# Optimization experiments

Measured on AMD Instinct MI355X. Metric: run time of the kernel, lower is better.

The kernel has to match this reference:

```python
import jax, jax.numpy as jnp
import numpy as np

N = 100_000   # nodes
E = 200_000   # directed edges
G = 2_500     # graphs in batch
F_NODE = 16
F_EDGE = 8
H1 = 32
H2 = 16


def setup_inputs() -> dict:
    key = jax.random.key(0)
    ks = jax.random.split(key, 24)
    p = lambda k, shape: 0.1 * jax.random.normal(k, shape, dtype=jnp.float32)
    inp = {
        "x": jax.random.normal(ks[0], (N, F_NODE), dtype=jnp.float32),
        "edge_attr": jax.random.normal(ks[1], (E, F_EDGE), dtype=jnp.float32),
        # edge-MLP for conv1: F_EDGE -> 16 -> F_NODE*H1
        "w_e1a": p(ks[2], (F_EDGE, 16)), "b_e1a": p(ks[3], (16,)),
        "w_e1b": p(ks[4], (16, F_NODE * H1)), "b_e1b": p(ks[5], (F_NODE * H1,)),
        "w_root1": p(ks[6], (F_NODE, H1)), "b_root1": p(ks[7], (H1,)),
        # edge-MLP for conv2: F_EDGE -> 16 -> H1*H2
        "w_e2a": p(ks[8], (F_EDGE, 16)), "b_e2a": p(ks[9], (16,)),
        "w_e2b": p(ks[10], (16, H1 * H2)), "b_e2b": p(ks[11], (H1 * H2,)),
        "w_root2": p(ks[12], (H1, H2)), "b_root2": p(ks[13], (H2,)),
        # attention-pool gate nn: F_NODE -> F_NODE -> 1
        "w_g1": p(ks[14], (F_NODE, F_NODE)), "b_g1": p(ks[15], (F_NODE,)),
        "w_g2": p(ks[16], (F_NODE, 1)), "b_g2": p(ks[17], (1,)),
        # head: (H2 + F_NODE) -> 8 -> 1
        "w_l1": p(ks[18], (H2 + F_NODE, 8)), "b_l1": p(ks[19], (8,)),
        "w_l2": p(ks[20], (8, 1)), "b_l2": p(ks[21], (1,)),
        "edge_index": jax.random.randint(ks[22], (2, E), 0, N),
        "batch": jnp.sort(jax.random.randint(ks[23], (N,), 0, G)),
    }
    return inp


def _nnconv(x, src, tgt, edge_attr, wa, ba, wb, bb, wr, br, in_c, out_c, n):
    # PyG NNConv: x_i' = x_i @ W_root + b + sum_{j->i} x_j @ Theta(e_ji)
    h = jax.nn.relu(edge_attr @ wa + ba)              # [E, 16]
    theta = (h @ wb + bb).reshape(-1, in_c, out_c)    # [E, in, out]
    msg = jnp.einsum('ei,eio->eo', x[src], theta)     # [E, out]
    agg = jax.ops.segment_sum(msg, tgt, num_segments=n)
    return x @ wr + br + agg


def reference(x, edge_attr, w_e1a, b_e1a, w_e1b, b_e1b, w_root1, b_root1,
              w_e2a, b_e2a, w_e2b, b_e2b, w_root2, b_root2,
              w_g1, b_g1, w_g2, b_g2, w_l1, b_l1, w_l2, b_l2,
              edge_index, batch):
    src, tgt = edge_index[0], edge_index[1]
    n = x.shape[0]

    # GlobalAttention pooling on raw node features (per-graph segment softmax)
    gate = jax.nn.relu(x @ w_g1 + b_g1) @ w_g2 + b_g2          # [N, 1]
    m = jax.ops.segment_max(gate, batch, num_segments=G)       # [G, 1]
    a = jnp.exp(gate - m[batch])
    s = jax.ops.segment_sum(a, batch, num_segments=G)
    x_att = jax.ops.segment_sum((a / s[batch]) * x, batch, num_segments=G)  # [G, F_NODE]

    # Two NNConv layers with ReLU
    h = jax.nn.relu(_nnconv(x, src, tgt, edge_attr, w_e1a, b_e1a, w_e1b, b_e1b,
                            w_root1, b_root1, F_NODE, H1, n))
    h = jax.nn.relu(_nnconv(h, src, tgt, edge_attr, w_e2a, b_e2a, w_e2b, b_e2b,
                            w_root2, b_root2, H1, H2, n))

    # global_mean_pool
    cnt = jax.ops.segment_sum(jnp.ones((n, 1), h.dtype), batch, num_segments=G)
    mean = jax.ops.segment_sum(h, batch, num_segments=G) / jnp.maximum(cnt, 1.0)

    z = jnp.concatenate([mean, x_att], axis=1)  # [G, H2 + F_NODE]
    # eval mode: dropout p=0.5 is identity; two linear layers, no activation between
    z = z @ w_l1 + b_l1
    z = z @ w_l2 + b_l2
    return z
```

## Files before the change

### kernel.cpp

```cpp
#include <hip/hip_runtime.h>
#include <hip/hip_bf16.h>

#define NN 100000
#define NE 200000
#define NG 2500
#define FN 16
#define FE 8
#define H1C 32
#define H2C 16
#define KH 16

typedef __attribute__((ext_vector_type(4))) float f32x4;
typedef _Float16 __attribute__((ext_vector_type(2))) half2v;
typedef _Float16 __attribute__((ext_vector_type(8))) half8v;
typedef __fp16 __attribute__((ext_vector_type(2))) pkf16x2;

__device__ __forceinline__ float bf2f(unsigned int u){
  union { unsigned int i; float f; } v; v.i = (u & 0xffffu) << 16; return v.f;
}
__device__ __forceinline__ unsigned int pkh(float a, float b){
  union { pkf16x2 h; unsigned int u; } v; v.h = __builtin_amdgcn_cvt_pkrtz(a, b); return v.u;
}
__device__ __forceinline__ float h2lo(unsigned int u){
  union { unsigned short s; _Float16 h; } v; v.s = (unsigned short)u; return (float)v.h;
}
__device__ __forceinline__ float h2hi(unsigned int u){
  union { unsigned short s; _Float16 h; } v; v.s = (unsigned short)(u >> 16); return (float)v.h;
}
__device__ __forceinline__ float rdf(const void* p, long i, bool isbf){
  return isbf ? bf2f(((const unsigned short*)p)[i]) : ((const float*)p)[i];
}
__device__ __forceinline__ void atomic_pk_f16(unsigned short* addr, unsigned int pk){
  asm volatile("global_atomic_pk_add_f16 %0, %1, off" :: "v"(addr), "v"(pk) : "memory");
}
__device__ __forceinline__ bool detect_isbf(const void* __restrict__ x){
  const unsigned short* u = (const unsigned short*)x;
  int lane = threadIdx.x & 63;
  float f = bf2f(u[2*lane]);
  float a = fabsf(f);
  bool sane = (f == 0.0f) || (a > 1e-4f && a < 1e4f);
  unsigned long long b = __ballot(sane);
  return __popcll(b) >= 32;
}
__device__ __forceinline__ void load_x16(const void* __restrict__ xin, bool isbf, int n, float* xv){
  if(isbf){
    uint4 u0 = ((const uint4*)xin)[2*n], u1 = ((const uint4*)xin)[2*n+1];
    xv[0]=bf2f(u0.x); xv[1]=bf2f(u0.x>>16); xv[2]=bf2f(u0.y); xv[3]=bf2f(u0.y>>16);
    xv[4]=bf2f(u0.z); xv[5]=bf2f(u0.z>>16); xv[6]=bf2f(u0.w); xv[7]=bf2f(u0.w>>16);
    xv[8]=bf2f(u1.x); xv[9]=bf2f(u1.x>>16); xv[10]=bf2f(u1.y); xv[11]=bf2f(u1.y>>16);
    xv[12]=bf2f(u1.z); xv[13]=bf2f(u1.z>>16); xv[14]=bf2f(u1.w); xv[15]=bf2f(u1.w>>16);
  } else {
    #pragma unroll
    for(int q = 0; q < 4; q++){
      float4 v = ((const float4*)xin)[4*n + q];
      xv[q*4+0]=v.x; xv[q*4+1]=v.y; xv[q*4+2]=v.z; xv[q*4+3]=v.w;
    }
  }
}

#define NW 20
struct WArgs { const void* p[NW]; };
enum {
  OW_E1A=0,     OB_E1A=128,   OW_E1B=144,   OB_E1B=8336,  OW_R1=8848,  OB_R1=9360,
  OW_E2A=9392,  OB_E2A=9520,  OW_E2B=9536,  OB_E2B=17728, OW_R2=18240, OB_R2=18752,
  OW_G1=18768,  OB_G1=19024,  OW_G2=19040,  OB_G2=19056,
  OW_L1=19057,  OB_L1=19313,  OW_L2=19321,  OB_L2=19329
};

template<int IN, int OUT, bool RAWX>
__device__ __forceinline__ void conv_tile(
    int u, const void* __restrict__ nodef, bool isbf,
    const unsigned int* __restrict__ hpk, const int* __restrict__ ei,
    const unsigned short* __restrict__ wpack, unsigned short* __restrict__ agg)
{
  constexpr int KMF  = ((KH*IN + IN + 31)/32)*32;
  constexpr int KP   = KMF + 8;
  constexpr int NT   = OUT/16;
  constexpr int KS   = KMF/32;
  int tid = threadIdx.x;
  int lane = tid & 63, m = lane & 15, quad = lane >> 4;
  int wid = tid >> 6;
  int ebase = u*64 + wid*16;
  int em = ebase + m;
  int sn = ei[em];
  int q1 = quad >> 1;
  int xoff = (IN == 16) ? ((quad & 1)*8) : (quad*8);
  union { half8v v; half2v h[4]; unsigned int w[4]; } X;
  if(RAWX){
    if(isbf){
      uint4 uu = *(const uint4*)((const unsigned short*)nodef + (size_t)sn*IN + xoff);
      X.w[0] = pkh(bf2f(uu.x), bf2f(uu.x >> 16));
      X.w[1] = pkh(bf2f(uu.y), bf2f(uu.y >> 16));
      X.w[2] = pkh(bf2f(uu.z), bf2f(uu.z >> 16));
      X.w[3] = pkh(bf2f(uu.w), bf2f(uu.w >> 16));
    } else {
      const float4* xp = (const float4*)((const float*)nodef + (size_t)sn*IN + xoff);
      float4 v0 = xp[0], v1 = xp[1];
      X.w[0] = pkh(v0.x, v0.y);
      X.w[1] = pkh(v0.z, v0.w);
      X.w[2] = pkh(v1.x, v1.y);
      X.w[3] = pkh(v1.z, v1.w);
    }
  } else {
    uint4 uu = *(const uint4*)((const unsigned short*)nodef + (size_t)sn*IN + xoff);
    X.w[0]=uu.x; X.w[1]=uu.y; X.w[2]=uu.z; X.w[3]=uu.w;
  }
  unsigned int hu[8];
  {
    const uint4* hp = (const uint4*)(hpk + (size_t)em*8);
    uint4 u0 = hp[0], u1 = hp[1];
    hu[0]=u0.x; hu[1]=u0.y; hu[2]=u0.z; hu[3]=u0.w;
    hu[4]=u1.x; hu[5]=u1.y; hu[6]=u1.z; hu[7]=u1.w;
  }
  int4 tg = *(const int4*)(ei + NE + ebase + quad*4);

  f32x4 acc[NT];
  #pragma unroll
  for(int nt = 0; nt < NT; nt++) acc[nt] = (f32x4){0.f,0.f,0.f,0.f};

  const half8v hz = {};
  #pragma unroll
  for(int ks = 0; ks < KS; ks++){
    union { half8v v; half2v h[4]; } A;
    if(ks < KS-1){
      unsigned short hs = (unsigned short)((IN == 16) ? (hu[ks] >> (16*q1))
                                                      : (hu[ks >> 1] >> (16*(ks & 1))));
      union { unsigned short s; _Float16 h; } hc; hc.s = hs;
      half2v hv2 = { hc.h, hc.h };
      #pragma unroll
      for(int k = 0; k < 4; k++) A.h[k] = hv2 * X.h[k];
    } else {
      if(IN == 16) A.v = (quad < 2) ? X.v : hz;
      else         A.v = X.v;
    }
    #pragma unroll
    for(int nt = 0; nt < NT; nt++){
      half8v b = *(const half8v*)(wpack + (size_t)(nt*16 + m)*KP + ks*32 + quad*8);
      acc[nt] = __builtin_amdgcn_mfma_f32_16x16x32_f16(A.v, b, acc[nt], 0, 0, 0);
    }
  }
  int tr[4] = {tg.x, tg.y, tg.z, tg.w};
  int mlo = m & ~1;
  bool evn = (m & 1) == 0;
  #pragma unroll
  for(int r = 0; r < 4; r++){
    #pragma unroll
    for(int nt = 0; nt < NT; nt++){
      float v = acc[nt][r];
      float vn = __shfl_xor(v, 1);
      if(evn ? (r < 2) : (r >= 2)){
        unsigned int pk = evn ? pkh(v, vn) : pkh(vn, v);
        atomic_pk_f16(agg + (size_t)tr[r]*OUT + nt*16 + mlo, pk);
      }
    }
  }
}

#define MB_A 76
#define MB_B (MB_A + 19)
#define MB_C (MB_B + 18)
#define MB_D (MB_C + 391)
#define MB_E (MB_D + 782)
#define MB_F (MB_E + 391)
__global__ void __launch_bounds__(256) mega1_kernel(
    const void* __restrict__ xin, const void* __restrict__ efin, WArgs w,
    const int* __restrict__ batch,
    float* __restrict__ wts, unsigned int* __restrict__ wpack1, unsigned int* __restrict__ wpack2,
    float* __restrict__ gate,
    unsigned int* __restrict__ hpk1,
    int* __restrict__ gstart, unsigned short* __restrict__ agg1)
{
  int b = blockIdx.x, tid = threadIdx.x;
  if(b < MB_A){
    bool isbf = detect_isbf(xin);
    int i = b*256 + tid;
    if(i >= 19330) return;
    const int sz[NW] = {128,16,8192,512,512,32, 128,16,8192,512,512,16, 256,16,16,1, 256,8,8,1};
    int seg = 0; long base = 0;
    while(i - base >= sz[seg]){ base += sz[seg]; seg++; }
    wts[i] = rdf(w.p[seg], i - base, isbf);
    return;
  }
  if(b < MB_B){
    bool isbf = detect_isbf(xin);
    int j = (b - MB_A)*256 + tid;
    if(j >= 4736) return;
    int n = j / 148; int k = (j % 148) * 2;
    float v0 = 0.f, v1 = 0.f;
    if(k < 256)        v0 = rdf(w.p[2], (long)k*32 + n, isbf);
    else if(k < 272)   v0 = rdf(w.p[3], (long)(k-256)*32 + n, isbf);
    if(k+1 < 256)      v1 = rdf(w.p[2], (long)(k+1)*32 + n, isbf);
    else if(k+1 < 272) v1 = rdf(w.p[3], (long)(k+1-256)*32 + n, isbf);
    wpack1[j] = pkh(v0, v1);
    return;
  }
  if(b < MB_C){
    bool isbf = detect_isbf(xin);
    int j = (b - MB_B)*256 + tid;
    if(j >= 4416) return;
    int n = j / 276; int k = (j % 276) * 2;
    float v0 = 0.f, v1 = 0.f;
    if(k < 512)        v0 = rdf(w.p[8], (long)k*16 + n, isbf);
    else if(k < 544)   v0 = rdf(w.p[9], (long)(k-512)*16 + n, isbf);
    if(k+1 < 512)      v1 = rdf(w.p[8], (long)(k+1)*16 + n, isbf);
    else if(k+1 < 544) v1 = rdf(w.p[9], (long)(k+1-512)*16 + n, isbf);
    wpack2[j] = pkh(v0, v1);
    return;
  }
  if(b < MB_D){
    __shared__ float s_w1[FN*FN], s_b1[FN], s_w2[FN], s_b2v[1];
    bool isbf = detect_isbf(xin);
    if(tid < FN*FN) s_w1[tid] = rdf(w.p[12], tid, isbf);
    if(tid < FN){ s_b1[tid] = rdf(w.p[13], tid, isbf); s_w2[tid] = rdf(w.p[14], tid, isbf); }
    if(tid == 0) s_b2v[0] = rdf(w.p[15], 0, isbf);
    __syncthreads();
    int n = (b - MB_C)*256 + tid;
    if(n >= NN) return;
    {
      int b1 = batch[n];
      int b0 = (n == 0) ? -1 : batch[n-1];
      for(int g2 = b0 + 1; g2 <= b1; g2++) gstart[g2] = n;
      if(n == NN-1) for(int g2 = b1 + 1; g2 <= NG; g2++) gstart[g2] = NN;
    }
    float xv[FN];
    load_x16(xin, isbf, n, xv);
    float g = s_b2v[0];
    #pragma unroll
    for(int j = 0; j < FN; j++){
      float hj = s_b1[j];
      #pragma unroll
      for(int i = 0; i < FN; i++) hj += xv[i] * s_w1[i*FN + j];
      hj = hj > 0.f ? hj : 0.f;
      g += hj * s_w2[j];
    }
    gate[n] = g;
    return;
  }
  if(b < MB_E){
    __shared__ float s_w1[FE*KH], s_b1[KH];
    bool isbf = detect_isbf(xin);
    if(tid < FE*KH) s_w1[tid] = rdf(w.p[0], tid, isbf);
    if(tid < KH) s_b1[tid] = rdf(w.p[1], tid, isbf);
    __syncthreads();
    int e = (b - MB_D)*256 + tid;
    if(e >= NE) return;
    float ev[FE];
    if(isbf){
      uint4 u = ((const uint4*)efin)[e];
      ev[0]=bf2f(u.x); ev[1]=bf2f(u.x>>16); ev[2]=bf2f(u.y); ev[3]=bf2f(u.y>>16);
      ev[4]=bf2f(u.z); ev[5]=bf2f(u.z>>16); ev[6]=bf2f(u.w); ev[7]=bf2f(u.w>>16);
    } else {
      float4 a = ((const float4*)efin)[2*e], bb = ((const float4*)efin)[2*e+1];
      ev[0]=a.x; ev[1]=a.y; ev[2]=a.z; ev[3]=a.w; ev[4]=bb.x; ev[5]=bb.y; ev[6]=bb.z; ev[7]=bb.w;
    }
    unsigned int o[8];
    #pragma unroll
    for(int d = 0; d < 8; d++){
      float h0 = s_b1[2*d], h1 = s_b1[2*d+1];
      #pragma unroll
      for(int k = 0; k < FE; k++){
        h0 += ev[k] * s_w1[k*KH + 2*d];
        h1 += ev[k] * s_w1[k*KH + 2*d+1];
      }
      h0 = h0 > 0.f ? h0 : 0.f; h1 = h1 > 0.f ? h1 : 0.f;
      o[d] = pkh(h0, h1);
    }
    uint4* p1 = (uint4*)(hpk1 + (size_t)e*8);
    p1[0] = make_uint4(o[0],o[1],o[2],o[3]); p1[1] = make_uint4(o[4],o[5],o[6],o[7]);
    return;
  }
  {
    int idx = (b - MB_E)*256 + tid;
    if(idx < 100000){
      uint4 z = make_uint4(0,0,0,0);
      uint4* p = (uint4*)((char*)agg1 + (size_t)idx*64);
      p[0] = z; p[1] = z; p[2] = z; p[3] = z;
    }
  }
}

#define C1_CONV (NE/64)
#define C1_E2   (C1_CONV + 782)
#define C1_Z    (C1_E2 + 196)
#define C1_ATT  (C1_Z + 625)
__global__ void __launch_bounds__(256) conv1_kernel(
    const void* __restrict__ xin, const void* __restrict__ efin,
    const float* __restrict__ wts,
    const unsigned int* __restrict__ hpk1, const int* __restrict__ ei,
    const unsigned short* __restrict__ wpack1,
    unsigned short* __restrict__ agg1, unsigned short* __restrict__ agg2,
    unsigned int* __restrict__ hpk2,
    const float* __restrict__ gate, const int* __restrict__ gstart,
    float* __restrict__ xatt)
{
  int b = blockIdx.x, tid = threadIdx.x;
  bool isbf = detect_isbf(xin);
  if(b < C1_CONV){
    conv_tile<FN, H1C, true>(b, xin, isbf, hpk1, ei, wpack1, agg1);
    return;
  }
  if(b < C1_E2){
    __shared__ float s_w2[FE*KH], s_b2[KH];
    if(tid < FE*KH) s_w2[tid] = wts[OW_E2A + tid];
    if(tid < KH) s_b2[tid] = wts[OB_E2A + tid];
    __syncthreads();
    int e = (b - C1_CONV)*256 + tid;
    if(e >= NE) return;
    float ev[FE];
    if(isbf){
      uint4 u = ((const uint4*)efin)[e];
      ev[0]=bf2f(u.x); ev[1]=bf2f(u.x>>16); ev[2]=bf2f(u.y); ev[3]=bf2f(u.y>>16);
      ev[4]=bf2f(u.z); ev[5]=bf2f(u.z>>16); ev[6]=bf2f(u.w); ev[7]=bf2f(u.w>>16);
    } else {
      float4 a = ((const float4*)efin)[2*e], bb = ((const float4*)efin)[2*e+1];
      ev[0]=a.x; ev[1]=a.y; ev[2]=a.z; ev[3]=a.w; ev[4]=bb.x; ev[5]=bb.y; ev[6]=bb.z; ev[7]=bb.w;
    }
    unsigned int o[8];
    #pragma unroll
    for(int d = 0; d < 8; d++){
      float h0 = s_b2[2*d], h1 = s_b2[2*d+1];
      #pragma unroll
      for(int k = 0; k < FE; k++){
        h0 += ev[k] * s_w2[k*KH + 2*d];
        h1 += ev[k] * s_w2[k*KH + 2*d+1];
      }
      h0 = h0 > 0.f ? h0 : 0.f; h1 = h1 > 0.f ? h1 : 0.f;
      o[d] = pkh(h0, h1);
    }
    uint4* p2 = (uint4*)(hpk2 + (size_t)e*8);
    p2[0] = make_uint4(o[0],o[1],o[2],o[3]); p2[1] = make_uint4(o[4],o[5],o[6],o[7]);
    return;
  }
  if(b < C1_Z){
    int idx = (b - C1_E2)*256 + tid;
    if(idx < 50000){
      uint4 z = make_uint4(0,0,0,0);
      uint4* p = (uint4*)((char*)agg2 + (size_t)idx*64);
      p[0] = z; p[1] = z; p[2] = z; p[3] = z;
    }
    return;
  }
  {
    int lane = tid & 63, wid = tid >> 6;
    int g = (b - C1_Z)*4 + wid;
    int start = gstart[g], end = gstart[g+1];
    float mx = -1e30f;
    for(int n = start + lane; n < end; n += 64) mx = fmaxf(mx, gate[n]);
    #pragma unroll
    for(int o = 32; o >= 1; o >>= 1) mx = fmaxf(mx, __shfl_xor(mx, o));
    float s = 0.f;
    float acc[FN];
    #pragma unroll
    for(int f = 0; f < FN; f++) acc[f] = 0.f;
    for(int n = start + lane; n < end; n += 64){
      float a = __expf(gate[n] - mx);
      s += a;
      float xv[FN];
      load_x16(xin, isbf, n, xv);
      #pragma unroll
      for(int f = 0; f < FN; f++) acc[f] += a * xv[f];
    }
    #pragma unroll
    for(int o = 32; o >= 1; o >>= 1){
      s += __shfl_xor(s, o);
      #pragma unroll
      for(int f = 0; f < FN; f++) acc[f] += __shfl_xor(acc[f], o);
    }
    if(lane < FN) xatt[(size_t)g*FN + lane] = (end > start && s > 0.f) ? acc[lane] / s : 0.f;
  }
}

__global__ void __launch_bounds__(256) conv2_kernel(
    const unsigned short* __restrict__ h1b, const unsigned int* __restrict__ hpk2,
    const int* __restrict__ ei, const unsigned short* __restrict__ wpack2,
    unsigned short* __restrict__ agg2)
{
  conv_tile<H1C, H2C, false>(blockIdx.x, h1b, false, hpk2, ei, wpack2, agg2);
}

__global__ void __launch_bounds__(256) node1_kernel(
    const void* __restrict__ xin, const unsigned short* __restrict__ agg1,
    const float* __restrict__ wr, const float* __restrict__ br,
    unsigned short* __restrict__ h1b)
{
  __shared__ float s_w[FN*H1C], s_b[H1C];
  for(int i = threadIdx.x; i < FN*H1C; i += 256) s_w[i] = wr[i];
  if(threadIdx.x < H1C) s_b[threadIdx.x] = br[threadIdx.x];
  bool isbf = detect_isbf(xin);
  __syncthreads();
  int g = blockIdx.x*256 + threadIdx.x;
  int n = g >> 3, q = g & 7;
  if(n >= NN) return;
  uint2 au = *(const uint2*)(agg1 + (size_t)n*H1C + q*4);
  float a0 = s_b[q*4+0] + h2lo(au.x), a1 = s_b[q*4+1] + h2hi(au.x);
  float a2 = s_b[q*4+2] + h2lo(au.y), a3 = s_b[q*4+3] + h2hi(au.y);
  float xv[FN];
  load_x16(xin, isbf, n, xv);
  #pragma unroll
  for(int i = 0; i < FN; i++){
    float xi = xv[i];
    a0 += xi*s_w[i*H1C + q*4+0]; a1 += xi*s_w[i*H1C + q*4+1];
    a2 += xi*s_w[i*H1C + q*4+2]; a3 += xi*s_w[i*H1C + q*4+3];
  }
  a0 = a0>0.f?a0:0.f; a1 = a1>0.f?a1:0.f; a2 = a2>0.f?a2:0.f; a3 = a3>0.f?a3:0.f;
  uint2 hb; hb.x = pkh(a0, a1); hb.y = pkh(a2, a3);
  *(uint2*)(h1b + (size_t)n*H1C + q*4) = hb;
}

__global__ void __launch_bounds__(256) node2_kernel(
    const unsigned short* __restrict__ h1b, const unsigned short* __restrict__ agg2,
    const float* __restrict__ wr, const float* __restrict__ br, float* __restrict__ h2)
{
  __shared__ float s_w[H1C*H2C], s_b[H2C];
  for(int i = threadIdx.x; i < H1C*H2C; i += 256) s_w[i] = wr[i];
  if(threadIdx.x < H2C) s_b[threadIdx.x] = br[threadIdx.x];
  __syncthreads();
  int g = blockIdx.x*256 + threadIdx.x;
  int n = g >> 2, q = g & 3;
  if(n >= NN) return;
  uint2 au = *(const uint2*)(agg2 + (size_t)n*H2C + q*4);
  float a0 = s_b[q*4+0] + h2lo(au.x), a1 = s_b[q*4+1] + h2hi(au.x);
  float a2 = s_b[q*4+2] + h2lo(au.y), a3 = s_b[q*4+3] + h2hi(au.y);
  const unsigned int* hb = (const unsigned int*)(h1b + (size_t)n*H1C);
  #pragma unroll
  for(int i2 = 0; i2 < H1C/2; i2++){
    unsigned int u = hb[i2];
    float x0 = h2lo(u), x1 = h2hi(u);
    int i = 2*i2;
    a0 += x0*s_w[i*H2C + q*4+0] + x1*s_w[(i+1)*H2C + q*4+0];
    a1 += x0*s_w[i*H2C + q*4+1] + x1*s_w[(i+1)*H2C + q*4+1];
    a2 += x0*s_w[i*H2C + q*4+2] + x1*s_w[(i+1)*H2C + q*4+2];
    a3 += x0*s_w[i*H2C + q*4+3] + x1*s_w[(i+1)*H2C + q*4+3];
  }
  float4 r; r.x = a0>0.f?a0:0.f; r.y = a1>0.f?a1:0.f; r.z = a2>0.f?a2:0.f; r.w = a3>0.f?a3:0.f;
  *(float4*)(h2 + (size_t)n*H2C + q*4) = r;
}

__global__ void head_kernel(const float* __restrict__ xatt,
    const float* __restrict__ h2, const int* __restrict__ gstart, const void* __restrict__ xin,
    const float* __restrict__ wl1, const float* __restrict__ bl1,
    const float* __restrict__ wl2, const float* __restrict__ bl2,
    void* __restrict__ out)
{
  __shared__ float sz[H2C + FN];
  int g = blockIdx.x;
  int lane = threadIdx.x;
  bool isbf = detect_isbf(xin);
  int start = gstart[g];
  int end   = gstart[g + 1];
  float acc[H2C];
  #pragma unroll
  for(int f = 0; f < H2C; f++) acc[f] = 0.f;
  for(int n = start + lane; n < end; n += 64){
    const float4* hp = (const float4*)(h2 + (size_t)n*H2C);
    #pragma unroll
    for(int q = 0; q < 4; q++){
      float4 v = hp[q];
      acc[q*4+0] += v.x; acc[q*4+1] += v.y; acc[q*4+2] += v.z; acc[q*4+3] += v.w;
    }
  }
  #pragma unroll
  for(int o = 32; o >= 1; o >>= 1){
    #pragma unroll
    for(int f = 0; f < H2C; f++) acc[f] += __shfl_xor(acc[f], o);
  }
  float inv = 1.f / fmaxf((float)(end - start), 1.f);
  if(lane < H2C) sz[lane] = acc[lane] * inv;
  if(lane < FN)  sz[H2C + lane] = xatt[(size_t)g*FN + lane];
  __syncthreads();
  if(lane == 0){
    float t1[8];
    #pragma unroll
    for(int j = 0; j < 8; j++){
      float t = bl1[j];
      #pragma unroll
      for(int c = 0; c < H2C + FN; c++) t += sz[c] * wl1[c*8 + j];
      t1[j] = t;
    }
    float o = bl2[0];
    #pragma unroll
    for(int j = 0; j < 8; j++) o += t1[j] * wl2[j];
    if(isbf) ((__hip_bfloat16*)out)[g] = __float2bfloat16(o);
    else     ((float*)out)[g] = o;
  }
}

extern "C" void kernel_launch(void* const* d_in, const int* in_sizes, int n_in,
                              void* d_out, int out_size, void* d_ws, size_t ws_size,
                              hipStream_t stream)
{
  const int* ei    = (const int*)d_in[22];
  const int* batch = (const int*)d_in[23];

  float* ws = (float*)d_ws;
  float* gate   = ws;
  float* wts    = gate + 100000;
  float* xatt   = wts + 19360;
  int*   gstart = (int*)(xatt + 40000);
  unsigned int* wpack1 = (unsigned int*)(gstart + 2504);
  unsigned int* wpack2 = wpack1 + 4736;
  unsigned int* hpk1   = wpack2 + 4416;
  unsigned int* hpk2   = hpk1 + 1600000;
  unsigned short* h1b  = (unsigned short*)(hpk2 + 1600000);
  float* h2     = (float*)(h1b + 3200000);
  unsigned short* agg1 = (unsigned short*)(h2 + 1600000);
  unsigned short* agg2 = agg1 + 3200000;

  WArgs wa;
  for(int i = 0; i < NW; i++) wa.p[i] = d_in[2 + i];

  mega1_kernel<<<MB_F, 256, 0, stream>>>(d_in[0], d_in[1], wa, batch,
      wts, wpack1, wpack2, gate, hpk1, gstart, agg1);

  conv1_kernel<<<C1_ATT, 256, 0, stream>>>(d_in[0], d_in[1], wts, hpk1, ei,
      (const unsigned short*)wpack1, agg1, agg2, hpk2, gate, gstart, xatt);
  node1_kernel<<<(NN*8 + 255)/256, 256, 0, stream>>>(d_in[0], agg1, wts+OW_R1, wts+OB_R1, h1b);

  conv2_kernel<<<NE/64, 256, 0, stream>>>(h1b, hpk2, ei,
      (const unsigned short*)wpack2, agg2);
  node2_kernel<<<(NN*4 + 255)/256, 256, 0, stream>>>(h1b, agg2, wts+OW_R2, wts+OB_R2, h2);

  head_kernel<<<NG, 64, 0, stream>>>(xatt, h2, gstart, d_in[0],
      wts+OW_L1, wts+OB_L1, wts+OW_L2, wts+OB_L2, d_out);
}
```

Baseline: 185.0 us.

## Fuse node-update kernels into conv2 gather and head pooling

Removes the node1 and node2 kernels. conv2 now recomputes the layer-1 node update (root linear, bias, ReLU) for each source node it gathers, using raw x and agg1. The head kernel recomputes both node updates per node during mean pooling and handles four graphs per block. This cuts two launches and the h1b/h2 intermediate buffers, at the price of redundant per-edge and per-node arithmetic and larger register use.

```diff
diff --git a/kernel.cpp b/kernel.cpp
--- a/kernel.cpp
+++ b/kernel.cpp
@@ -66,95 +66,6 @@
   OW_G1=18768,  OB_G1=19024,  OW_G2=19040,  OB_G2=19056,
   OW_L1=19057,  OB_L1=19313,  OW_L2=19321,  OB_L2=19329
 };
-
-template<int IN, int OUT, bool RAWX>
-__device__ __forceinline__ void conv_tile(
-    int u, const void* __restrict__ nodef, bool isbf,
-    const unsigned int* __restrict__ hpk, const int* __restrict__ ei,
-    const unsigned short* __restrict__ wpack, unsigned short* __restrict__ agg)
-{
-  constexpr int KMF  = ((KH*IN + IN + 31)/32)*32;
-  constexpr int KP   = KMF + 8;
-  constexpr int NT   = OUT/16;
-  constexpr int KS   = KMF/32;
-  int tid = threadIdx.x;
-  int lane = tid & 63, m = lane & 15, quad = lane >> 4;
-  int wid = tid >> 6;
-  int ebase = u*64 + wid*16;
-  int em = ebase + m;
-  int sn = ei[em];
-  int q1 = quad >> 1;
-  int xoff = (IN == 16) ? ((quad & 1)*8) : (quad*8);
-  union { half8v v; half2v h[4]; unsigned int w[4]; } X;
-  if(RAWX){
-    if(isbf){
-      uint4 uu = *(const uint4*)((const unsigned short*)nodef + (size_t)sn*IN + xoff);
-      X.w[0] = pkh(bf2f(uu.x), bf2f(uu.x >> 16));
-      X.w[1] = pkh(bf2f(uu.y), bf2f(uu.y >> 16));
-      X.w[2] = pkh(bf2f(uu.z), bf2f(uu.z >> 16));
-      X.w[3] = pkh(bf2f(uu.w), bf2f(uu.w >> 16));
-    } else {
-      const float4* xp = (const float4*)((const float*)nodef + (size_t)sn*IN + xoff);
-      float4 v0 = xp[0], v1 = xp[1];
-      X.w[0] = pkh(v0.x, v0.y);
-      X.w[1] = pkh(v0.z, v0.w);
-      X.w[2] = pkh(v1.x, v1.y);
-      X.w[3] = pkh(v1.z, v1.w);
-    }
-  } else {
-    uint4 uu = *(const uint4*)((const unsigned short*)nodef + (size_t)sn*IN + xoff);
-    X.w[0]=uu.x; X.w[1]=uu.y; X.w[2]=uu.z; X.w[3]=uu.w;
-  }
-  unsigned int hu[8];
-  {
-    const uint4* hp = (const uint4*)(hpk + (size_t)em*8);
-    uint4 u0 = hp[0], u1 = hp[1];
-    hu[0]=u0.x; hu[1]=u0.y; hu[2]=u0.z; hu[3]=u0.w;
-    hu[4]=u1.x; hu[5]=u1.y; hu[6]=u1.z; hu[7]=u1.w;
-  }
-  int4 tg = *(const int4*)(ei + NE + ebase + quad*4);
-
-  f32x4 acc[NT];
-  #pragma unroll
-  for(int nt = 0; nt < NT; nt++) acc[nt] = (f32x4){0.f,0.f,0.f,0.f};
-
-  const half8v hz = {};
-  #pragma unroll
-  for(int ks = 0; ks < KS; ks++){
-    union { half8v v; half2v h[4]; } A;
-    if(ks < KS-1){
-      unsigned short hs = (unsigned short)((IN == 16) ? (hu[ks] >> (16*q1))
-                                                      : (hu[ks >> 1] >> (16*(ks & 1))));
-      union { unsigned short s; _Float16 h; } hc; hc.s = hs;
-      half2v hv2 = { hc.h, hc.h };
-      #pragma unroll
-      for(int k = 0; k < 4; k++) A.h[k] = hv2 * X.h[k];
-    } else {
-      if(IN == 16) A.v = (quad < 2) ? X.v : hz;
-      else         A.v = X.v;
-    }
-    #pragma unroll
-    for(int nt = 0; nt < NT; nt++){
-      half8v b = *(const half8v*)(wpack + (size_t)(nt*16 + m)*KP + ks*32 + quad*8);
-      acc[nt] = __builtin_amdgcn_mfma_f32_16x16x32_f16(A.v, b, acc[nt], 0, 0, 0);
-    }
-  }
-  int tr[4] = {tg.x, tg.y, tg.z, tg.w};
-  int mlo = m & ~1;
-  bool evn = (m & 1) == 0;
-  #pragma unroll
-  for(int r = 0; r < 4; r++){
-    #pragma unroll
-    for(int nt = 0; nt < NT; nt++){
-      float v = acc[nt][r];
-      float vn = __shfl_xor(v, 1);
-      if(evn ? (r < 2) : (r >= 2)){
-        unsigned int pk = evn ? pkh(v, vn) : pkh(vn, v);
-        atomic_pk_f16(agg + (size_t)tr[r]*OUT + nt*16 + mlo, pk);
-      }
-    }
-  }
-}
 
 #define MB_A 76
 #define MB_B (MB_A + 19)
@@ -287,7 +198,7 @@
     const void* __restrict__ xin, const void* __restrict__ efin,
     const float* __restrict__ wts,
     const unsigned int* __restrict__ hpk1, const int* __restrict__ ei,
-    const unsigned short* __restrict__ wpack1,
+    const unsigned short* __restrict__ wpack,
     unsigned short* __restrict__ agg1, unsigned short* __restrict__ agg2,
     unsigned int* __restrict__ hpk2,
     const float* __restrict__ gate, const int* __restrict__ gstart,
@@ -296,7 +207,75 @@
   int b = blockIdx.x, tid = threadIdx.x;
   bool isbf = detect_isbf(xin);
   if(b < C1_CONV){
-    conv_tile<FN, H1C, true>(b, xin, isbf, hpk1, ei, wpack1, agg1);
+    constexpr int IN = FN, OUT = H1C;
+    constexpr int KMF = 288, KP = 296, NT = 2, KS = 9;
+    int lane = tid & 63, m = lane & 15, quad = lane >> 4;
+    int wid = tid >> 6;
+    int ebase = b*64 + wid*16;
+    int em = ebase + m;
+    int sn = ei[em];
+    int q1 = quad >> 1;
+    int xoff = (quad & 1)*8;
+    union { half8v v; half2v h[4]; unsigned int w[4]; } X;
+    if(isbf){
+      uint4 uu = *(const uint4*)((const unsigned short*)xin + (size_t)sn*IN + xoff);
+      X.w[0] = pkh(bf2f(uu.x), bf2f(uu.x >> 16));
+      X.w[1] = pkh(bf2f(uu.y), bf2f(uu.y >> 16));
+      X.w[2] = pkh(bf2f(uu.z), bf2f(uu.z >> 16));
+      X.w[3] = pkh(bf2f(uu.w), bf2f(uu.w >> 16));
+    } else {
+      const float4* xp = (const float4*)((const float*)xin + (size_t)sn*IN + xoff);
+      float4 v0 = xp[0], v1 = xp[1];
+      X.w[0] = pkh(v0.x, v0.y);
+      X.w[1] = pkh(v0.z, v0.w);
+      X.w[2] = pkh(v1.x, v1.y);
+      X.w[3] = pkh(v1.z, v1.w);
+    }
+    unsigned int hu[8];
+    {
+      const uint4* hp = (const uint4*)(hpk1 + (size_t)em*8);
+      uint4 u0 = hp[0], u1 = hp[1];
+      hu[0]=u0.x; hu[1]=u0.y; hu[2]=u0.z; hu[3]=u0.w;
+      hu[4]=u1.x; hu[5]=u1.y; hu[6]=u1.z; hu[7]=u1.w;
+    }
+    int4 tg = *(const int4*)(ei + NE + ebase + quad*4);
+    f32x4 acc[NT];
+    #pragma unroll
+    for(int nt = 0; nt < NT; nt++) acc[nt] = (f32x4){0.f,0.f,0.f,0.f};
+    const half8v hz = {};
+    #pragma unroll
+    for(int ks = 0; ks < KS; ks++){
+      union { half8v v; half2v h[4]; } A;
+      if(ks < KS-1){
+        unsigned short hs = (unsigned short)(hu[ks] >> (16*q1));
+        union { unsigned short s; _Float16 h; } hc; hc.s = hs;
+        half2v hv2 = { hc.h, hc.h };
+        #pragma unroll
+        for(int k = 0; k < 4; k++) A.h[k] = hv2 * X.h[k];
+      } else {
+        A.v = (quad < 2) ? X.v : hz;
+      }
+      #pragma unroll
+      for(int nt = 0; nt < NT; nt++){
+        half8v bb = *(const half8v*)(wpack + (size_t)(nt*16 + m)*KP + ks*32 + quad*8);
+        acc[nt] = __builtin_amdgcn_mfma_f32_16x16x32_f16(A.v, bb, acc[nt], 0, 0, 0);
+      }
+    }
+    int tr[4] = {tg.x, tg.y, tg.z, tg.w};
+    int mlo = m & ~1;
+    bool evn = (m & 1) == 0;
+    #pragma unroll
+    for(int r = 0; r < 4; r++){
+      #pragma unroll
+      for(int nt = 0; nt < NT; nt++){
+        float v = acc[nt][r];
+        float vn = __shfl_xor(v, 1);
+        if(evn ? (r < 2) : (r >= 2)){
+          unsigned int pk = evn ? pkh(v, vn) : pkh(vn, v);
+          atomic_pk_f16(agg1 + (size_t)tr[r]*H1C + nt*16 + mlo, pk);
+        }
+      }
+    }
     return;
   }
   if(b < C1_E2){
@@ -371,93 +350,153 @@
 }
 
 __global__ void __launch_bounds__(256) conv2_kernel(
-    const unsigned short* __restrict__ h1b, const unsigned int* __restrict__ hpk2,
-    const int* __restrict__ ei, const unsigned short* __restrict__ wpack2,
-    unsigned short* __restrict__ agg2)
+    const void* __restrict__ xin, const unsigned short* __restrict__ agg1,
+    const float* __restrict__ wts,
+    const unsigned int* __restrict__ hpk2, const int* __restrict__ ei,
+    const unsigned short* __restrict__ wpack, unsigned short* __restrict__ agg2)
 {
-  conv_tile<H1C, H2C, false>(blockIdx.x, h1b, false, hpk2, ei, wpack2, agg2);
-}
-
-__global__ void __launch_bounds__(256) node1_kernel(
-    const void* __restrict__ xin, const unsigned short* __restrict__ agg1,
-    const float* __restrict__ wr, const float* __restrict__ br,
-    unsigned short* __restrict__ h1b)
-{
+  constexpr int KP = 552, KS = 17;
   __shared__ float s_w[FN*H1C], s_b[H1C];
-  for(int i = threadIdx.x; i < FN*H1C; i += 256) s_w[i] = wr[i];
-  if(threadIdx.x < H1C) s_b[threadIdx.x] = br[threadIdx.x];
+  int tid = threadIdx.x;
+  for(int i = tid; i < FN*H1C; i += 256) s_w[i] = wts[OW_R1 + i];
+  if(tid < H1C) s_b[tid] = wts[OB_R1 + tid];
   bool isbf = detect_isbf(xin);
   __syncthreads();
-  int g = blockIdx.x*256 + threadIdx.x;
-  int n = g >> 3, q = g & 7;
-  if(n >= NN) return;
-  uint2 au = *(const uint2*)(agg1 + (size_t)n*H1C + q*4);
-  float a0 = s_b[q*4+0] + h2lo(au.x), a1 = s_b[q*4+1] + h2hi(au.x);
-  float a2 = s_b[q*4+2] + h2lo(au.y), a3 = s_b[q*4+3] + h2hi(au.y);
+  int lane = tid & 63, m = lane & 15, quad = lane >> 4;
+  int wid = tid >> 6;
+  int ebase = blockIdx.x*64 + wid*16;
+  int em = ebase + m;
+  int sn = ei[em];
+  int xoff = quad*8;
   float xv[FN];
-  load_x16(xin, isbf, n, xv);
+  load_x16(xin, isbf, sn, xv);
+  uint4 au = *(const uint4*)(agg1 + (size_t)sn*H1C + xoff);
+  float hv[8];
+  hv[0]=h2lo(au.x); hv[1]=h2hi(au.x); hv[2]=h2lo(au.y); hv[3]=h2hi(au.y);
+  hv[4]=h2lo(au.z); hv[5]=h2hi(au.z); hv[6]=h2lo(au.w); hv[7]=h2hi(au.w);
+  #pragma unroll
+  for(int t = 0; t < 8; t++) hv[t] += s_b[xoff + t];
   #pragma unroll
   for(int i = 0; i < FN; i++){
     float xi = xv[i];
-    a0 += xi*s_w[i*H1C + q*4+0]; a1 += xi*s_w[i*H1C + q*4+1];
-    a2 += xi*s_w[i*H1C + q*4+2]; a3 += xi*s_w[i*H1C + q*4+3];
-  }
-  a0 = a0>0.f?a0:0.f; a1 = a1>0.f?a1:0.f; a2 = a2>0.f?a2:0.f; a3 = a3>0.f?a3:0.f;
-  uint2 hb; hb.x = pkh(a0, a1); hb.y = pkh(a2, a3);
-  *(uint2*)(h1b + (size_t)n*H1C + q*4) = hb;
-}
-
-__global__ void __launch_bounds__(256) node2_kernel(
-    const unsigned short* __restrict__ h1b, const unsigned short* __restrict__ agg2,
-    const float* __restrict__ wr, const float* __restrict__ br, float* __restrict__ h2)
-{
-  __shared__ float s_w[H1C*H2C], s_b[H2C];
-  for(int i = threadIdx.x; i < H1C*H2C; i += 256) s_w[i] = wr[i];
-  if(threadIdx.x < H2C) s_b[threadIdx.x] = br[threadIdx.x];
-  __syncthreads();
-  int g = blockIdx.x*256 + threadIdx.x;
-  int n = g >> 2, q = g & 3;
-  if(n >= NN) return;
-  uint2 au = *(const uint2*)(agg2 + (size_t)n*H2C + q*4);
-  float a0 = s_b[q*4+0] + h2lo(au.x), a1 = s_b[q*4+1] + h2hi(au.x);
-  float a2 = s_b[q*4+2] + h2lo(au.y), a3 = s_b[q*4+3] + h2hi(au.y);
-  const unsigned int* hb = (const unsigned int*)(h1b + (size_t)n*H1C);
-  #pragma unroll
-  for(int i2 = 0; i2 < H1C/2; i2++){
-    unsigned int u = hb[i2];
-    float x0 = h2lo(u), x1 = h2hi(u);
-    int i = 2*i2;
-    a0 += x0*s_w[i*H2C + q*4+0] + x1*s_w[(i+1)*H2C + q*4+0];
-    a1 += x0*s_w[i*H2C + q*4+1] + x1*s_w[(i+1)*H2C + q*4+1];
-    a2 += x0*s_w[i*H2C + q*4+2] + x1*s_w[(i+1)*H2C + q*4+2];
-    a3 += x0*s_w[i*H2C + q*4+3] + x1*s_w[(i+1)*H2C + q*4+3];
-  }
-  float4 r; r.x = a0>0.f?a0:0.f; r.y = a1>0.f?a1:0.f; r.z = a2>0.f?a2:0.f; r.w = a3>0.f?a3:0.f;
-  *(float4*)(h2 + (size_t)n*H2C + q*4) = r;
-}
-
-__global__ void head_kernel(const float* __restrict__ xatt,
-    const float* __restrict__ h2, const int* __restrict__ gstart, const void* __restrict__ xin,
-    const float* __restrict__ wl1, const float* __restrict__ bl1,
-    const float* __restrict__ wl2, const float* __restrict__ bl2,
+    #pragma unroll
+    for(int t = 0; t < 8; t++) hv[t] += xi * s_w[i*H1C + xoff + t];
+  }
+  union { half8v v; half2v h[4]; unsigned int w[4]; } X;
+  #pragma unroll
+  for(int k = 0; k < 4; k++){
+    float a = hv[2*k]   > 0.f ? hv[2*k]   : 0.f;
+    float b = hv[2*k+1] > 0.f ? hv[2*k+1] : 0.f;
+    X.w[k] = pkh(a, b);
+  }
+  unsigned int hu[8];
+  {
+    const uint4* hp = (const uint4*)(hpk2 + (size_t)em*8);
+    uint4 u0 = hp[0], u1 = hp[1];
+    hu[0]=u0.x; hu[1]=u0.y; hu[2]=u0.z; hu[3]=u0.w;
+    hu[4]=u1.x; hu[5]=u1.y; hu[6]=u1.z; hu[7]=u1.w;
+  }
+  int4 tg = *(const int4*)(ei + NE + ebase + quad*4);
+  f32x4 acc = (f32x4){0.f,0.f,0.f,0.f};
+  #pragma unroll
+  for(int ks = 0; ks < KS; ks++){
+    union { half8v v; half2v h[4]; } A;
+    if(ks < KS-1){
+      unsigned short hs = (unsigned short)(hu[ks >> 1] >> (16*(ks & 1)));
+      union { unsigned short s; _Float16 h; } hc; hc.s = hs;
+      half2v hv2 = { hc.h, hc.h };
+      #pragma unroll
+      for(int k = 0; k < 4; k++) A.h[k] = hv2 * X.h[k];
+    } else {
+      A.v = X.v;
+    }
+    half8v bb = *(const half8v*)(wpack + (size_t)m*KP + ks*32 + quad*8);
+    acc = __builtin_amdgcn_mfma_f32_16x16x32_f16(A.v, bb, acc, 0, 0, 0);
+  }
+  int tr[4] = {tg.x, tg.y, tg.z, tg.w};
+  int mlo = m & ~1;
+  bool evn = (m & 1) == 0;
+  #pragma unroll
+  for(int r = 0; r < 4; r++){
+    float v = acc[r];
+    float vn = __shfl_xor(v, 1);
+    if(evn ? (r < 2) : (r >= 2)){
+      unsigned int pk = evn ? pkh(v, vn) : pkh(vn, v);
+      atomic_pk_f16(agg2 + (size_t)tr[r]*H2C + mlo, pk);
+    }
+  }
+}
+
+__global__ void __launch_bounds__(256) head_kernel(
+    const void* __restrict__ xin, const unsigned short* __restrict__ agg1,
+    const unsigned short* __restrict__ agg2, const float* __restrict__ xatt,
+    const int* __restrict__ gstart, const float* __restrict__ wts,
     void* __restrict__ out)
 {
-  __shared__ float sz[H2C + FN];
-  int g = blockIdx.x;
-  int lane = threadIdx.x;
+  __shared__ float s_w1[FN*H1C], s_b1[H1C], s_w2[H1C*H2C], s_b2[H2C];
+  __shared__ float s_l1[(H2C+FN)*8], s_lb1[8], s_l2[8], s_lb2[1];
+  __shared__ float sz[4][H2C+FN];
+  int tid = threadIdx.x;
+  for(int i = tid; i < FN*H1C; i += 256){ s_w1[i] = wts[OW_R1+i]; s_w2[i] = wts[OW_R2+i]; }
+  if(tid < H1C) s_b1[tid] = wts[OB_R1+tid];
+  if(tid < H2C) s_b2[tid] = wts[OB_R2+tid];
+  s_l1[tid] = wts[OW_L1 + tid];
+  if(tid < 8){ s_lb1[tid] = wts[OB_L1+tid]; s_l2[tid] = wts[OW_L2+tid]; }
+  if(tid == 0) s_lb2[0] = wts[OB_L2];
   bool isbf = detect_isbf(xin);
-  int start = gstart[g];
-  int end   = gstart[g + 1];
+  __syncthreads();
+  int lane = tid & 63, wid = tid >> 6;
+  int g = blockIdx.x*4 + wid;
+  int start = gstart[g], end = gstart[g+1];
   float acc[H2C];
   #pragma unroll
   for(int f = 0; f < H2C; f++) acc[f] = 0.f;
   for(int n = start + lane; n < end; n += 64){
-    const float4* hp = (const float4*)(h2 + (size_t)n*H2C);
-    #pragma unroll
-    for(int q = 0; q < 4; q++){
-      float4 v = hp[q];
-      acc[q*4+0] += v.x; acc[q*4+1] += v.y; acc[q*4+2] += v.z; acc[q*4+3] += v.w;
-    }
+    float xv[FN];
+    load_x16(xin, isbf, n, xv);
+    float h1[H1C];
+    {
+      const uint4* ap = (const uint4*)(agg1 + (size_t)n*H1C);
+      uint4 a0 = ap[0], a1 = ap[1], a2 = ap[2], a3 = ap[3];
+      unsigned int aw[16] = {a0.x,a0.y,a0.z,a0.w, a1.x,a1.y,a1.z,a1.w,
+                             a2.x,a2.y,a2.z,a2.w, a3.x,a3.y,a3.z,a3.w};
+      #pragma unroll
+      for(int c2 = 0; c2 < 16; c2++){ h1[2*c2] = h2lo(aw[c2]); h1[2*c2+1] = h2hi(aw[c2]); }
+    }
+    #pragma unroll
+    for(int c = 0; c < H1C; c++) h1[c] += s_b1[c];
+    #pragma unroll
+    for(int i = 0; i < FN; i++){
+      float xi = xv[i];
+      #pragma unroll
+      for(int c = 0; c < H1C; c++) h1[c] += xi * s_w1[i*H1C + c];
+    }
+    #pragma unroll
+    for(int c2 = 0; c2 < 16; c2++){
+      float a = h1[2*c2]   > 0.f ? h1[2*c2]   : 0.f;
+      float b = h1[2*c2+1] > 0.f ? h1[2*c2+1] : 0.f;
+      unsigned int u = pkh(a, b);
+      h1[2*c2] = h2lo(u); h1[2*c2+1] = h2hi(u);
+    }
+    float hv2[H2C];
+    {
+      const uint4* bp = (const uint4*)(agg2 + (size_t)n*H2C);
+      uint4 b0 = bp[0], b1 = bp[1];
+      unsigned int bw[8] = {b0.x,b0.y,b0.z,b0.w, b1.x,b1.y,b1.z,b1.w};
+      #pragma unroll
+      for(int o2 = 0; o2 < 8; o2++){ hv2[2*o2] = h2lo(bw[o2]); hv2[2*o2+1] = h2hi(bw[o2]); }
+    }
+    #pragma unroll
+    for(int o = 0; o < H2C; o++) hv2[o] += s_b2[o];
+    #pragma unroll
+    for(int i2 = 0; i2 < H1C/2; i2++){
+      float x0 = h1[2*i2], x1 = h1[2*i2+1];
+      #pragma unroll
+      for(int o = 0; o < H2C; o++)
+        hv2[o] += x0*s_w2[2*i2*H2C + o] + x1*s_w2[(2*i2+1)*H2C + o];
+    }
+    #pragma unroll
+    for(int o = 0; o < H2C; o++) acc[o] += (hv2[o] > 0.f ? hv2[o] : 0.f);
   }
   #pragma unroll
   for(int o = 32; o >= 1; o >>= 1){
@@ -465,21 +504,21 @@
     for(int f = 0; f < H2C; f++) acc[f] += __shfl_xor(acc[f], o);
   }
   float inv = 1.f / fmaxf((float)(end - start), 1.f);
-  if(lane < H2C) sz[lane] = acc[lane] * inv;
-  if(lane < FN)  sz[H2C + lane] = xatt[(size_t)g*FN + lane];
+  if(lane < H2C) sz[wid][lane] = acc[lane] * inv;
+  if(lane < FN)  sz[wid][H2C + lane] = xatt[(size_t)g*FN + lane];
   __syncthreads();
   if(lane == 0){
     float t1[8];
     #pragma unroll
     for(int j = 0; j < 8; j++){
-      float t = bl1[j];
-      #pragma unroll
-      for(int c = 0; c < H2C + FN; c++) t += sz[c] * wl1[c*8 + j];
+      float t = s_lb1[j];
+      #pragma unroll
+      for(int c = 0; c < H2C + FN; c++) t += sz[wid][c] * s_l1[c*8 + j];
       t1[j] = t;
     }
-    float o = bl2[0];
-    #pragma unroll
-    for(int j = 0; j < 8; j++) o += t1[j] * wl2[j];
+    float o = s_lb2[0];
+    #pragma unroll
+    for(int j = 0; j < 8; j++) o += t1[j] * s_l2[j];
     if(isbf) ((__hip_bfloat16*)out)[g] = __float2bfloat16(o);
     else     ((float*)out)[g] = o;
   }
@@ -501,9 +540,7 @@
   unsigned int* wpack2 = wpack1 + 4736;
   unsigned int* hpk1   = wpack2 + 4416;
   unsigned int* hpk2   = hpk1 + 1600000;
-  unsigned short* h1b  = (unsigned short*)(hpk2 + 1600000);
-  float* h2     = (float*)(h1b + 3200000);
-  unsigned short* agg1 = (unsigned short*)(h2 + 1600000);
+  unsigned short* agg1 = (unsigned short*)(hpk2 + 1600000);
   unsigned short* agg2 = agg1 + 3200000;
 
   WArgs wa;
@@ -514,12 +551,9 @@
 
   conv1_kernel<<<C1_ATT, 256, 0, stream>>>(d_in[0], d_in[1], wts, hpk1, ei,
       (const unsigned short*)wpack1, agg1, agg2, hpk2, gate, gstart, xatt);
-  node1_kernel<<<(NN*8 + 255)/256, 256, 0, stream>>>(d_in[0], agg1, wts+OW_R1, wts+OB_R1, h1b);
-
-  conv2_kernel<<<NE/64, 256, 0, stream>>>(h1b, hpk2, ei,
+
+  conv2_kernel<<<NE/64, 256, 0, stream>>>(d_in[0], agg1, wts, hpk2, ei,
       (const unsigned short*)wpack2, agg2);
-  node2_kernel<<<(NN*4 + 255)/256, 256, 0, stream>>>(h1b, agg2, wts+OW_R2, wts+OB_R2, h2);
-
-  head_kernel<<<NG, 64, 0, stream>>>(xatt, h2, gstart, d_in[0],
-      wts+OW_L1, wts+OB_L1, wts+OW_L2, wts+OB_L2, d_out);
-}
+
+  head_kernel<<<NG/4, 256, 0, stream>>>(d_in[0], agg1, agg2, xatt, gstart, wts, d_out);
+}
```

Result: slower. 644.5 us (+248.4%).
